# Kernel tuning notes

Measured on AMD Instinct MI355X. Metric: run time of the kernel, lower is better.

The kernel has to match this reference:

```python
import jax, jax.numpy as jnp
import numpy as np

D_MODEL = 1024
NUM_HEADS = 16
D_K = D_MODEL // NUM_HEADS
B, S = 4, 2048
NEG_INF = -1e9


def _linear_params(key, d_out, d_in):
    k1, k2 = jax.random.split(key)
    lim = 1.0 / np.sqrt(d_in)
    w = jax.random.uniform(k1, (d_out, d_in), jnp.float32, -lim, lim)
    b = jax.random.uniform(k2, (d_out,), jnp.float32, -lim, lim)
    return w, b


def setup_inputs() -> dict:
    key = jax.random.key(0)
    ks = jax.random.split(key, 16)
    query = jax.random.normal(ks[0], (B, S, D_MODEL), jnp.float32)
    kk = jax.random.normal(ks[1], (B, S, D_MODEL), jnp.float32)
    vv = jax.random.normal(ks[2], (B, S, D_MODEL), jnp.float32)
    # causal mask, broadcastable to [B,H,Sq,Sk]
    mask = jnp.tril(jnp.ones((S, S), jnp.int32))[None, None]
    wq1, bq1 = _linear_params(ks[3], D_MODEL, D_MODEL)
    wq2, bq2 = _linear_params(ks[4], D_MODEL, D_MODEL)
    wk1, bk1 = _linear_params(ks[5], D_MODEL, D_MODEL)
    wk2, bk2 = _linear_params(ks[6], D_MODEL, D_MODEL)
    wv1, bv1 = _linear_params(ks[7], D_MODEL, D_MODEL)
    wv2, bv2 = _linear_params(ks[8], D_MODEL, D_MODEL)
    wo, bo = _linear_params(ks[9], D_MODEL, D_MODEL)
    return dict(query=query, key=kk, value=vv, mask=mask,
                wq1=wq1, bq1=bq1, wq2=wq2, bq2=bq2,
                wk1=wk1, bk1=bk1, wk2=wk2, bk2=bk2,
                wv1=wv1, bv1=bv1, wv2=wv2, bv2=bv2,
                wo=wo, bo=bo)


def _swiglu_proj(x, w1, b1, w2, b2):
    # F.silu(w1(x)) * w2(x)
    return jax.nn.silu(x @ w1.T + b1) * (x @ w2.T + b2)


def _split_heads(x):
    b, s, _ = x.shape
    return x.reshape(b, s, NUM_HEADS, D_K).transpose(0, 2, 1, 3)  # [B,H,S,dk]


def reference(query, key, value, mask,
              wq1, bq1, wq2, bq2,
              wk1, bk1, wk2, bk2,
              wv1, bv1, wv2, bv2,
              wo, bo):
    q = _split_heads(_swiglu_proj(query, wq1, bq1, wq2, bq2))
    k = _split_heads(_swiglu_proj(key, wk1, bk1, wk2, bk2))
    v = _split_heads(_swiglu_proj(value, wv1, bv1, wv2, bv2))
    scores = jnp.einsum('bhqd,bhkd->bhqk', q, k) / np.sqrt(D_K).astype(np.float32)
    scores = jnp.where(mask == 0, jnp.float32(NEG_INF), scores)
    attn = jax.nn.softmax(scores, axis=-1)
    x = jnp.einsum('bhqk,bhkd->bhqd', attn, v)  # [B,H,S,dk]
    x = x.transpose(0, 2, 1, 3).reshape(query.shape[0], -1, NUM_HEADS * D_K)
    return x @ wo.T + bo
```

## Files before the change

### kernel.cpp

```cpp
#include <hip/hip_runtime.h>


typedef __bf16 bf16;
typedef bf16 bf16x8 __attribute__((ext_vector_type(8)));
typedef float f32x4 __attribute__((ext_vector_type(4)));
typedef unsigned short u16;
typedef unsigned int u32;
typedef u16 u16x8 __attribute__((ext_vector_type(8)));
typedef u16 u16x4 __attribute__((ext_vector_type(4)));

#define DEVI static __device__ __forceinline__

DEVI u16 f2b(float f) {
  union { float f; u32 u; } v; v.f = f;
  u32 r = v.u + 0x7FFFu + ((v.u >> 16) & 1u);
  return (u16)(r >> 16);
}
DEVI f32x4 mfma16(bf16x8 a, bf16x8 b, f32x4 c) {
  return __builtin_amdgcn_mfma_f32_16x16x32_bf16(a, b, c, 0, 0, 0);
}
DEVI void gload16(const void* g, void* l) {
  __builtin_amdgcn_global_load_lds(
      (const __attribute__((address_space(1))) void*)g,
      (__attribute__((address_space(3))) void*)l, 16, 0, 0);
}
DEVI u32 cvtpk(float lo, float hi) {
  u32 r;
  asm("v_cvt_pk_bf16_f32 %0, %1, %2" : "=v"(r) : "v"(lo), "v"(hi));
  return r;
}
DEVI void pswap(u32& a, u32& b) {
  asm("v_permlane32_swap_b32 %0, %1" : "+v"(a), "+v"(b));
}

struct P6 { const float* p[6]; };

__global__ void cvt_wpair(P6 in, u16* __restrict__ out) {
  const int pair = blockIdx.y;
  const float* w1 = in.p[2 * pair];
  const float* w2 = in.p[2 * pair + 1];
  u16* dst = out + (size_t)pair * 2097152;
  const int i = blockIdx.x * 256 + threadIdx.x;
  const int v = i >> 7;
  const int k0 = (i & 127) << 3;
  const int t7 = v & 127;
  const int g = (t7 >> 4) & 1;
  const int c = (v >> 7) * 64 + ((t7 >> 5) << 4) + (t7 & 15);
  const float* src = (g ? w2 : w1) + (size_t)c * 1024 + k0;
  const f32x4 a = *(const f32x4*)src;
  const f32x4 b = *(const f32x4*)(src + 4);
  u16x8 wv;
#pragma unroll
  for (int j = 0; j < 4; ++j) { wv[j] = f2b(a[j]); wv[4 + j] = f2b(b[j]); }
  *(u16x8*)(dst + (size_t)v * 1024 + k0) = wv;
}

__global__ void cvt_x(const float* __restrict__ s0, u16* __restrict__ d0,
                      const float* __restrict__ s1, u16* __restrict__ d1) {
  const float* src = blockIdx.y ? s1 : s0;
  u16* dst = blockIdx.y ? d1 : d0;
  const int i = blockIdx.x * 256 + threadIdx.x;
  const f32x4 a = ((const f32x4*)src)[i * 2];
  const f32x4 b = ((const f32x4*)src)[i * 2 + 1];
  u16x8 w;
#pragma unroll
  for (int j = 0; j < 4; ++j) { w[j] = f2b(a[j]); w[4 + j] = f2b(b[j]); }
  ((u16x8*)dst)[i] = w;
}

struct GArgs {
  const u16* A; const u16* W;
  const float* b1; const float* b2;
  void* out; float scale;
};

template<int MODE, bool DUAL>
__global__ __launch_bounds__(256, 2) void gemm128(GArgs g0, GArgs g1)
{
  __shared__ char smem[65536];
  const int fl = blockIdx.x;
  const GArgs g = (DUAL && fl >= 1024) ? g1 : g0;
  const int local = DUAL ? (fl & 1023) : fl;
  const int t = threadIdx.x;
  const int lane = t & 63, wid = t >> 6;
  const int lg = lane >> 4, lc = lane & 15;
  const int wr = (wid >> 1) * 64, wc = (wid & 1) * 64;
  constexpr int NXB = (MODE == 2) ? 8 : 16;
  const int xcd = local & 7, w8 = local >> 3;
  const int m0 = (xcd * 8 + w8 / NXB) * 128;
  const int bx = w8 % NXB;
  const int K = 1024;
  const int srow = lane >> 3, scolb = (lane & 7) << 4;

  const f32x4 fz = {0.f, 0.f, 0.f, 0.f};
  f32x4 acc[4][4];
#pragma unroll
  for (int i = 0; i < 4; ++i)
#pragma unroll
    for (int j = 0; j < 4; ++j) acc[i][j] = fz;

  auto STAGE = [&](int buf, int kt) {
    const int k0 = kt << 6;
    char* As = smem + buf * 32768;
    char* Ws = As + 16384;
#pragma unroll
    for (int p = 0; p < 4; ++p) {
      const int rb = wid * 32 + p * 8;
      const int row = rb + srow;
      const int ce = (scolb ^ ((row & 7) << 4)) >> 1;
      gload16(g.A + (size_t)(m0 + row) * K + k0 + ce, As + rb * 128);
      gload16(g.W + (size_t)(bx * 128 + row) * K + k0 + ce, Ws + rb * 128);
    }
  };

  STAGE(0, 0);
  __syncthreads();
  for (int kt = 0; kt < 16; ++kt) {
    const int cur = kt & 1;
    if (kt < 15) STAGE(cur ^ 1, kt + 1);
    const char* As = smem + cur * 32768;
    const char* Ws = As + 16384;
#pragma unroll
    for (int kh = 0; kh < 2; ++kh) {
      bf16x8 af[4], bfr[4];
#pragma unroll
      for (int mf = 0; mf < 4; ++mf) {
        const int r = wr + mf * 16 + lc;
        af[mf] = *(const bf16x8*)(As + r * 128 + ((kh * 64 + (lg << 4)) ^ ((r & 7) << 4)));
      }
#pragma unroll
      for (int nf = 0; nf < 4; ++nf) {
        const int v = wc + nf * 16 + lc;
        bfr[nf] = *(const bf16x8*)(Ws + v * 128 + ((kh * 64 + (lg << 4)) ^ ((v & 7) << 4)));
      }
#pragma unroll
      for (int mf = 0; mf < 4; ++mf)
#pragma unroll
        for (int nf = 0; nf < 4; ++nf)
          acc[mf][nf] = mfma16(af[mf], bfr[nf], acc[mf][nf]);
    }
    __syncthreads();
  }
  if constexpr (MODE == 2) {
    float* Co = (float*)g.out;
#pragma unroll
    for (int mf = 0; mf < 4; ++mf)
#pragma unroll
      for (int nf = 0; nf < 4; ++nf) {
        const int r0 = m0 + wr + mf * 16 + (lg << 2);
        const int C = bx * 128 + wc + nf * 16 + lc;
        const float bv = g.b1[C];
#pragma unroll
        for (int j = 0; j < 4; ++j)
          Co[(size_t)(r0 + j) * 1024 + C] = acc[mf][nf][j] + bv;
      }
  } else {
    u16* Co = (u16*)g.out;
#pragma unroll
    for (int mf = 0; mf < 4; ++mf) {
      const int r0 = m0 + wr + mf * 16 + (lg << 2);
#pragma unroll
      for (int p = 0; p < 2; ++p) {
        const int C = bx * 64 + (wid & 1) * 32 + p * 16 + lc;
        const float b1v = g.b1[C], b2v = g.b2[C];
        const int h = C >> 6, d = C & 63;
        if constexpr (MODE == 0) {
#pragma unroll
          for (int j = 0; j < 4; ++j) {
            const int r = r0 + j;
            const float x = acc[mf][2 * p][j] + b1v;
            const float y = acc[mf][2 * p + 1][j] + b2v;
            const float vv = (x / (1.f + __expf(-x))) * y * g.scale;
            const int bb = r >> 11, s = r & 2047;
            Co[((size_t)(bb * 16 + h) * 2048 + s) * 64 + d] = f2b(vv);
          }
        } else {
          u16x4 wv;
#pragma unroll
          for (int j = 0; j < 4; ++j) {
            const float x = acc[mf][2 * p][j] + b1v;
            const float y = acc[mf][2 * p + 1][j] + b2v;
            wv[j] = f2b((x / (1.f + __expf(-x))) * y);
          }
          const int bb = r0 >> 11, s0 = r0 & 2047;
          *(u16x4*)(Co + ((size_t)(bb * 16 + h) * 64 + d) * 2048 + s0) = wv;
        }
      }
    }
  }
}

__global__ __launch_bounds__(256, 4) void attn_fwd(
    const u16* __restrict__ Q, const u16* __restrict__ Kk,
    const u16* __restrict__ Vt, u16* __restrict__ O)
{
  __shared__ char smem[32768];
  const int t = threadIdx.x;
  const int lane = t & 63, wid = t >> 6;
  const int lg = lane >> 4, lc = lane & 15;
  const int flat = blockIdx.x;
  const int bh = flat & 63;
  const int qc = 15 - (flat >> 6);
  const int b = bh >> 4, h = bh & 15;
  const f32x4 fz = {0.f, 0.f, 0.f, 0.f};
  const float THR = 11.5f;
  const bool ev = ((lg & 1) == 0);

  auto STAGE = [&](int buf, int kt) {
    const int kbase = kt << 6;
    char* Kb = smem + buf * 16384;
    char* Vb = Kb + 8192;
#pragma unroll
    for (int p = 0; p < 4; ++p) {
      const int idx = wid * 4 + p;
      const int rb = (idx & 7) * 8;
      const int row = rb + (lane >> 3);
      const int ce = (((lane & 7) << 4) ^ ((row & 7) << 4)) >> 1;
      if (idx < 8)
        gload16(Kk + ((size_t)bh * 2048 + kbase + row) * 64 + ce, Kb + rb * 128);
      else
        gload16(Vt + ((size_t)bh * 64 + row) * 2048 + kbase + ce, Vb + rb * 128);
    }
  };

  const int qw = qc * 128 + wid * 32;

  bf16x8 qf[2][2];
#pragma unroll
  for (int qg = 0; qg < 2; ++qg)
#pragma unroll
    for (int kh = 0; kh < 2; ++kh)
      qf[qg][kh] = *(const bf16x8*)(Q + ((size_t)bh * 2048 + qw + qg * 16 + lc) * 64 + kh * 32 + lg * 8);

  f32x4 o[2][4];
#pragma unroll
  for (int qg = 0; qg < 2; ++qg)
#pragma unroll
    for (int dn = 0; dn < 4; ++dn) o[qg][dn] = fz;
  float mrow[2] = {-1e30f, -1e30f}, lsum[2] = {0.f, 0.f};

  const int nt = 2 * qc + 2;
  STAGE(0, 0);
  __syncthreads();
  for (int kt = 0; kt < nt; ++kt) {
    const int cur = kt & 1;
    if (kt + 1 < nt) STAGE(cur ^ 1, kt + 1);
    const int kbase = kt << 6;
    const char* Ks = smem + cur * 16384;
    const char* Vs = Ks + 8192;
    if (kbase <= qw + 31) {
      f32x4 sfT[4][2];
#pragma unroll
      for (int nf = 0; nf < 4; ++nf)
#pragma unroll
        for (int qg = 0; qg < 2; ++qg) sfT[nf][qg] = fz;
      __builtin_amdgcn_s_setprio(1);
#pragma unroll
      for (int kh = 0; kh < 2; ++kh) {
        bf16x8 kb[4];
#pragma unroll
        for (int nf = 0; nf < 4; ++nf) {
          const int r = nf * 16 + lc;
          kb[nf] = *(const bf16x8*)(Ks + r * 128 + ((kh * 64 + (lg << 4)) ^ ((r & 7) << 4)));
        }
#pragma unroll
        for (int nf = 0; nf < 4; ++nf) {
          sfT[nf][0] = mfma16(kb[nf], qf[0][kh], sfT[nf][0]);
          sfT[nf][1] = mfma16(kb[nf], qf[1][kh], sfT[nf][1]);
        }
      }
      __builtin_amdgcn_s_setprio(0);
      if (kbase + 63 > qw) {
#pragma unroll
        for (int qg = 0; qg < 2; ++qg) {
          const int qq = qw + qg * 16 + lc;
#pragma unroll
          for (int nf = 0; nf < 4; ++nf)
#pragma unroll
            for (int j = 0; j < 4; ++j)
              if (kbase + nf * 16 + (lg << 2) + j > qq) sfT[nf][qg][j] = -1e30f;
        }
      }
      float pm[2];
#pragma unroll
      for (int qg = 0; qg < 2; ++qg) {
        float m = sfT[0][qg][0];
#pragma unroll
        for (int nf = 0; nf < 4; ++nf)
#pragma unroll
          for (int j = 0; j < 4; ++j) m = fmaxf(m, sfT[nf][qg][j]);
        m = fmaxf(m, __shfl_xor(m, 16));
        m = fmaxf(m, __shfl_xor(m, 32));
        pm[qg] = m;
      }
      const bool ok = (pm[0] <= mrow[0] + THR) && (pm[1] <= mrow[1] + THR);
      if (!__all(ok)) {
#pragma unroll
        for (int qg = 0; qg < 2; ++qg) {
          const float mn = fmaxf(mrow[qg], pm[qg]);
          const float sc = exp2f(mrow[qg] - mn);
          mrow[qg] = mn;
          lsum[qg] *= sc;
#pragma unroll
          for (int dn = 0; dn < 4; ++dn)
#pragma unroll
            for (int j = 0; j < 4; ++j) o[qg][dn][j] *= sc;
        }
      }
#pragma unroll
      for (int qg = 0; qg < 2; ++qg)
#pragma unroll
        for (int nf = 0; nf < 4; ++nf)
#pragma unroll
          for (int j = 0; j < 4; ++j) {
            const float p = exp2f(sfT[nf][qg][j] - mrow[qg]);
            sfT[nf][qg][j] = p;
            lsum[qg] += p;
          }
      u32 pw[2][2][4];
#pragma unroll
      for (int qg = 0; qg < 2; ++qg)
#pragma unroll
        for (int kh = 0; kh < 2; ++kh) {
          u32 A0 = cvtpk(sfT[2 * kh][qg][0], sfT[2 * kh][qg][1]);
          u32 A1 = cvtpk(sfT[2 * kh][qg][2], sfT[2 * kh][qg][3]);
          u32 B0 = cvtpk(sfT[2 * kh + 1][qg][0], sfT[2 * kh + 1][qg][1]);
          u32 B1 = cvtpk(sfT[2 * kh + 1][qg][2], sfT[2 * kh + 1][qg][3]);
          pswap(A0, B0);
          pswap(A1, B1);
          const u32 P0s = __shfl_xor(A0, 16);
          const u32 Q0s = __shfl_xor(B0, 16);
          const u32 P1s = __shfl_xor(A1, 16);
          const u32 Q1s = __shfl_xor(B1, 16);
          pw[qg][kh][0] = ev ? A0 : Q0s;
          pw[qg][kh][1] = ev ? A1 : Q1s;
          pw[qg][kh][2] = ev ? P0s : B0;
          pw[qg][kh][3] = ev ? P1s : B1;
        }
      __builtin_amdgcn_s_setprio(1);
#pragma unroll
      for (int kh = 0; kh < 2; ++kh) {
        union { u32 u[4]; bf16x8 v; } p0, p1;
#pragma unroll
        for (int w = 0; w < 4; ++w) { p0.u[w] = pw[0][kh][w]; p1.u[w] = pw[1][kh][w]; }
#pragma unroll
        for (int dn = 0; dn < 4; ++dn) {
          const int vr = dn * 16 + lc;
          const bf16x8 vb = *(const bf16x8*)(Vs + vr * 128 + ((kh * 64 + (lg << 4)) ^ ((vr & 7) << 4)));
          o[0][dn] = mfma16(vb, p0.v, o[0][dn]);
          o[1][dn] = mfma16(vb, p1.v, o[1][dn]);
        }
      }
      __builtin_amdgcn_s_setprio(0);
    }
    __syncthreads();
  }
#pragma unroll
  for (int qg = 0; qg < 2; ++qg) {
    float l = lsum[qg];
    l += __shfl_xor(l, 16);
    l += __shfl_xor(l, 32);
    const float inv = __builtin_amdgcn_rcpf(l);
    const size_t ob = ((size_t)(b * 2048 + qw + qg * 16 + lc) * 16 + h) * 64 + (lg << 2);
#pragma unroll
    for (int dn = 0; dn < 4; ++dn) {
      u16x4 wv;
#pragma unroll
      for (int j = 0; j < 4; ++j) wv[j] = f2b(o[qg][dn][j] * inv);
      *(u16x4*)(O + ob + dn * 16) = wv;
    }
  }
}

extern "C" void kernel_launch(void* const* d_in, const int* in_sizes, int n_in,
                              void* d_out, int out_size, void* d_ws, size_t ws_size,
                              hipStream_t stream)
{
  (void)in_sizes; (void)n_in; (void)out_size; (void)ws_size;
  const float* xq  = (const float*)d_in[0];
  const float* xk  = (const float*)d_in[1];
  const float* xv  = (const float*)d_in[2];
  const float* wq1 = (const float*)d_in[4];
  const float* bq1 = (const float*)d_in[5];
  const float* wq2 = (const float*)d_in[6];
  const float* bq2 = (const float*)d_in[7];
  const float* wk1 = (const float*)d_in[8];
  const float* bk1 = (const float*)d_in[9];
  const float* wk2 = (const float*)d_in[10];
  const float* bk2 = (const float*)d_in[11];
  const float* wv1 = (const float*)d_in[12];
  const float* bv1 = (const float*)d_in[13];
  const float* wv2 = (const float*)d_in[14];
  const float* bv2 = (const float*)d_in[15];
  const float* wo  = (const float*)d_in[16];
  const float* bo  = (const float*)d_in[17];

  char* ws = (char*)d_ws;
  u16* WB = (u16*)ws;
  u16* XQ = (u16*)(ws + 14680064);
  u16* XK = (u16*)(ws + 31457280);
  u16* QB = (u16*)(ws + 48234496);
  u16* KB = (u16*)(ws + 65011712);
  u16* VT = (u16*)(ws + 81788928);
  u16* XV = XQ;
  u16* AO = XK;
  u16* WCQ = WB;
  u16* WCK = WB + 2097152;
  u16* WCV = WB + 4194304;
  u16* WO  = WB + 6291456;

  P6 p6 = {{wq1, wq2, wk1, wk2, wv1, wv2}};
  cvt_wpair<<<dim3(1024, 3), 256, 0, stream>>>(p6, WB);
  cvt_x<<<dim3(512, 1), 256, 0, stream>>>(wo, WO, wo, WO);
  cvt_x<<<dim3(4096, 2), 256, 0, stream>>>(xq, XQ, xk, XK);

  const float QSCALE = 0.125f * 1.44269504088896f;
  GArgs gq = {XQ, WCQ, bq1, bq2, QB, QSCALE};
  GArgs gk = {XK, WCK, bk1, bk2, KB, 1.0f};
  gemm128<0, true><<<2048, 256, 0, stream>>>(gq, gk);

  cvt_x<<<dim3(4096, 1), 256, 0, stream>>>(xv, XV, xv, XV);
  GArgs gv = {XV, WCV, bv1, bv2, VT, 1.0f};
  gemm128<1, false><<<1024, 256, 0, stream>>>(gv, gv);

  attn_fwd<<<1024, 256, 0, stream>>>(QB, KB, VT, AO);

  GArgs go = {AO, WO, bo, nullptr, d_out, 1.0f};
  gemm128<2, false><<<512, 256, 0, stream>>>(go, go);
}
```

Baseline: 237.5 us.

## Merge conversion kernels and fuse Q/K/V projection GEMMs into one launch

All fp32-to-bf16 conversions (weights, Wo, and the three inputs) now run in a single mega_cvt kernel. The Q, K and V SwiGLU projection GEMMs run in one 3072-block launch, with the epilogue mode chosen at runtime. This removes several kernel launches and lets the V GEMM overlap with Q/K instead of waiting on a separate conversion. To free workspace for the extra buffer, the bf16 copy of V is staged in the output buffer, and the epilogue mode is now a runtime branch rather than a template constant.

```diff
diff --git a/kernel.cpp b/kernel.cpp
--- a/kernel.cpp
+++ b/kernel.cpp
@@ -33,33 +33,13 @@
   asm("v_permlane32_swap_b32 %0, %1" : "+v"(a), "+v"(b));
 }
 
-struct P6 { const float* p[6]; };
-
-__global__ void cvt_wpair(P6 in, u16* __restrict__ out) {
-  const int pair = blockIdx.y;
-  const float* w1 = in.p[2 * pair];
-  const float* w2 = in.p[2 * pair + 1];
-  u16* dst = out + (size_t)pair * 2097152;
-  const int i = blockIdx.x * 256 + threadIdx.x;
-  const int v = i >> 7;
-  const int k0 = (i & 127) << 3;
-  const int t7 = v & 127;
-  const int g = (t7 >> 4) & 1;
-  const int c = (v >> 7) * 64 + ((t7 >> 5) << 4) + (t7 & 15);
-  const float* src = (g ? w2 : w1) + (size_t)c * 1024 + k0;
-  const f32x4 a = *(const f32x4*)src;
-  const f32x4 b = *(const f32x4*)(src + 4);
-  u16x8 wv;
-#pragma unroll
-  for (int j = 0; j < 4; ++j) { wv[j] = f2b(a[j]); wv[4 + j] = f2b(b[j]); }
-  *(u16x8*)(dst + (size_t)v * 1024 + k0) = wv;
-}
-
-__global__ void cvt_x(const float* __restrict__ s0, u16* __restrict__ d0,
-                      const float* __restrict__ s1, u16* __restrict__ d1) {
-  const float* src = blockIdx.y ? s1 : s0;
-  u16* dst = blockIdx.y ? d1 : d0;
-  const int i = blockIdx.x * 256 + threadIdx.x;
+struct CvtArgs {
+  const float* w[6];
+  const float* wo; const float* xq; const float* xk; const float* xv;
+  u16* WB; u16* WO; u16* XQ; u16* XK; u16* XV;
+};
+
+DEVI void cvt8(const float* __restrict__ src, u16* __restrict__ dst, int i) {
   const f32x4 a = ((const f32x4*)src)[i * 2];
   const f32x4 b = ((const f32x4*)src)[i * 2 + 1];
   u16x8 w;
@@ -68,24 +48,54 @@
   ((u16x8*)dst)[i] = w;
 }
 
+__global__ void mega_cvt(CvtArgs a) {
+  const int blk = blockIdx.x, t = threadIdx.x;
+  if (blk < 3072) {
+    const int pair = blk >> 10;
+    const int i = (blk & 1023) * 256 + t;
+    const float* w1 = a.w[2 * pair];
+    const float* w2 = a.w[2 * pair + 1];
+    u16* dst = a.WB + (size_t)pair * 2097152;
+    const int v = i >> 7;
+    const int k0 = (i & 127) << 3;
+    const int t7 = v & 127;
+    const int g = (t7 >> 4) & 1;
+    const int c = (v >> 7) * 64 + ((t7 >> 5) << 4) + (t7 & 15);
+    const float* src = (g ? w2 : w1) + (size_t)c * 1024 + k0;
+    const f32x4 x = *(const f32x4*)src;
+    const f32x4 y = *(const f32x4*)(src + 4);
+    u16x8 wv;
+#pragma unroll
+    for (int j = 0; j < 4; ++j) { wv[j] = f2b(x[j]); wv[4 + j] = f2b(y[j]); }
+    *(u16x8*)(dst + (size_t)v * 1024 + k0) = wv;
+  } else if (blk < 3584) {
+    cvt8(a.wo, a.WO, (blk - 3072) * 256 + t);
+  } else if (blk < 7680) {
+    cvt8(a.xq, a.XQ, (blk - 3584) * 256 + t);
+  } else if (blk < 11776) {
+    cvt8(a.xk, a.XK, (blk - 7680) * 256 + t);
+  } else {
+    cvt8(a.xv, a.XV, (blk - 11776) * 256 + t);
+  }
+}
+
 struct GArgs {
   const u16* A; const u16* W;
   const float* b1; const float* b2;
-  void* out; float scale;
+  void* out; float scale; int mode;
 };
 
-template<int MODE, bool DUAL>
-__global__ __launch_bounds__(256, 2) void gemm128(GArgs g0, GArgs g1)
+template<int NXB>
+__global__ __launch_bounds__(256, 2) void gemm128r(GArgs g0, GArgs g1, GArgs g2)
 {
   __shared__ char smem[65536];
   const int fl = blockIdx.x;
-  const GArgs g = (DUAL && fl >= 1024) ? g1 : g0;
-  const int local = DUAL ? (fl & 1023) : fl;
+  const GArgs g = (fl >= 2048) ? g2 : ((fl >= 1024) ? g1 : g0);
+  const int local = fl & 1023;
   const int t = threadIdx.x;
   const int lane = t & 63, wid = t >> 6;
   const int lg = lane >> 4, lc = lane & 15;
   const int wr = (wid >> 1) * 64, wc = (wid & 1) * 64;
-  constexpr int NXB = (MODE == 2) ? 8 : 16;
   const int xcd = local & 7, w8 = local >> 3;
   const int m0 = (xcd * 8 + w8 / NXB) * 128;
   const int bx = w8 % NXB;
@@ -141,7 +151,7 @@
     }
     __syncthreads();
   }
-  if constexpr (MODE == 2) {
+  if (g.mode == 2) {
     float* Co = (float*)g.out;
 #pragma unroll
     for (int mf = 0; mf < 4; ++mf)
@@ -164,7 +174,7 @@
         const int C = bx * 64 + (wid & 1) * 32 + p * 16 + lc;
         const float b1v = g.b1[C], b2v = g.b2[C];
         const int h = C >> 6, d = C & 63;
-        if constexpr (MODE == 0) {
+        if (g.mode == 0) {
 #pragma unroll
           for (int j = 0; j < 4; ++j) {
             const int r = r0 + j;
@@ -402,29 +412,28 @@
   u16* QB = (u16*)(ws + 48234496);
   u16* KB = (u16*)(ws + 65011712);
   u16* VT = (u16*)(ws + 81788928);
-  u16* XV = XQ;
+  u16* XV = (u16*)d_out;
   u16* AO = XK;
   u16* WCQ = WB;
   u16* WCK = WB + 2097152;
   u16* WCV = WB + 4194304;
   u16* WO  = WB + 6291456;
 
-  P6 p6 = {{wq1, wq2, wk1, wk2, wv1, wv2}};
-  cvt_wpair<<<dim3(1024, 3), 256, 0, stream>>>(p6, WB);
-  cvt_x<<<dim3(512, 1), 256, 0, stream>>>(wo, WO, wo, WO);
-  cvt_x<<<dim3(4096, 2), 256, 0, stream>>>(xq, XQ, xk, XK);
+  CvtArgs ca;
+  ca.w[0] = wq1; ca.w[1] = wq2; ca.w[2] = wk1;
+  ca.w[3] = wk2; ca.w[4] = wv1; ca.w[5] = wv2;
+  ca.wo = wo; ca.xq = xq; ca.xk = xk; ca.xv = xv;
+  ca.WB = WB; ca.WO = WO; ca.XQ = XQ; ca.XK = XK; ca.XV = XV;
+  mega_cvt<<<15872, 256, 0, stream>>>(ca);
 
   const float QSCALE = 0.125f * 1.44269504088896f;
-  GArgs gq = {XQ, WCQ, bq1, bq2, QB, QSCALE};
-  GArgs gk = {XK, WCK, bk1, bk2, KB, 1.0f};
-  gemm128<0, true><<<2048, 256, 0, stream>>>(gq, gk);
-
-  cvt_x<<<dim3(4096, 1), 256, 0, stream>>>(xv, XV, xv, XV);
-  GArgs gv = {XV, WCV, bv1, bv2, VT, 1.0f};
-  gemm128<1, false><<<1024, 256, 0, stream>>>(gv, gv);
+  GArgs gq = {XQ, WCQ, bq1, bq2, QB, QSCALE, 0};
+  GArgs gk = {XK, WCK, bk1, bk2, KB, 1.0f,   0};
+  GArgs gv = {XV, WCV, bv1, bv2, VT, 1.0f,   1};
+  gemm128r<16><<<3072, 256, 0, stream>>>(gq, gk, gv);
 
   attn_fwd<<<1024, 256, 0, stream>>>(QB, KB, VT, AO);
 
-  GArgs go = {AO, WO, bo, nullptr, d_out, 1.0f};
-  gemm128<2, false><<<512, 256, 0, stream>>>(go, go);
-}
+  GArgs go = {AO, WO, bo, nullptr, d_out, 1.0f, 2};
+  gemm128r<8><<<512, 256, 0, stream>>>(go, go, go);
+}
```

After: 234.2 us (median of 2 runs). Within noise of the previous version (-1.4%).
